# Optimization experiments

Hardware: AMD Instinct MI355X
Metric: run time of the kernel (lower is better)

The kernel has to match this reference:

```python
import jax, jax.numpy as jnp
import numpy as np

SHIFT = 1  # fixed instance of the random +/-1 shift_direction


def setup_inputs() -> dict:
    key = jax.random.key(0)
    k1, k2 = jax.random.split(key)
    x = jax.random.normal(k1, (128, 256, 28, 28), dtype=jnp.float32)
    W = jax.random.normal(k2, (128, 3, 128), dtype=jnp.float32)  # (j=in, k=3, i=out)
    return {"x": x, "W": W}


def reference(x, W):
    B, G, Cg, H, Wd = 128, 2, 128, 28, 28
    # view as (l, o, j, n, m) = (batch, group, chan, h, w)
    xg = x.reshape(B, G, Cg, H, Wd)
    # circular roll along width (original: roll(t, shift, dim=4))
    xg = jnp.roll(xg, SHIFT, axis=4)
    # unfold(3,1) pad (1,0) + einsum 'lojnmk, jki -> lonmi' is exactly a
    # zero-padded 1D conv along width with full channel mixing, shared over
    # group and h. Express it as a single grouped-batch conv.
    xm = xg.reshape(B * G, Cg, H, Wd)                 # (N, C, H, W)
    kern = jnp.transpose(W, (2, 0, 1))[:, :, None, :]  # (i, j, 1, 3) OIHW
    y = jax.lax.conv_general_dilated(
        xm, kern, window_strides=(1, 1), padding=((0, 0), (1, 1)),
        dimension_numbers=("NCHW", "OIHW", "NCHW"))   # (B*G, i, H, W)
    y = y.reshape(B, G, Cg, H, Wd)                    # (l, o, i, n, m)
    # second roll is along h (dim 1 of the (l,n,m,o*i) layout == n here)
    y = jnp.roll(y, SHIFT, axis=3)
    # final layout (l, o*i, n, m) == (128, 256, 28, 28)
    return y.reshape(B, G * Cg, H, Wd)
```

## Files before the change

kernel.cpp:

```cpp
#include <hip/hip_runtime.h>


typedef __bf16  bf16x8 __attribute__((ext_vector_type(8)));
typedef float  f32x16 __attribute__((ext_vector_type(16)));

__global__ __launch_bounds__(256, 2)
void shiftconv_kernel(const float* __restrict__ x,
                      const float* __restrict__ Wm,
                      float* __restrict__ out)
{
    __shared__ unsigned short xsp[34 * 128];

    const int tid  = threadIdx.x;
    const int wave = tid >> 6;
    const int lane = tid & 63;
    const int lo   = lane & 31;
    const int hi   = lane >> 5;

    const int b  = blockIdx.x;
    const int l  = b >> 3;
    const int o  = (b >> 2) & 1;
    const int nc = b & 3;

    bf16x8 bw[3][8];
    {
        const int i = wave * 32 + lo;
#pragma unroll
        for (int kw = 0; kw < 3; ++kw) {
#pragma unroll
            for (int jc = 0; jc < 8; ++jc) {
                const int j0 = jc * 16 + hi * 8;
#pragma unroll
                for (int e = 0; e < 8; ++e) {
                    bw[kw][jc][e] = (__bf16)Wm[(((j0 + e) * 3) + kw) * 128 + i];
                }
            }
        }
    }

    {
        const int rl[6] = {0, 29, 30, 31, 32, 33};
#pragma unroll
        for (int q = 0; q < 3; ++q) {
            const int e  = q * 256 + tid;
            const int rr = rl[e >> 7];
            const int j  = e & 127;
            xsp[rr * 128 + (j ^ ((rr & 7) << 3))] = 0;
        }
    }

    const float* xbase = x   + (size_t)(l * 256 + o * 128) * 784;
    float*       obase = out + (size_t)(l * 256 + o * 128) * 784;

    for (int n1 = nc * 7; n1 < nc * 7 + 7; ++n1) {
        __syncthreads();

        for (int g = tid; g < 896; g += 256) {
            const int j  = g / 7;
            const int mq = g - j * 7;
            const float4 v = *reinterpret_cast<const float4*>(
                xbase + j * 784 + n1 * 28 + mq * 4);
            const float vv[4] = {v.x, v.y, v.z, v.w};
#pragma unroll
            for (int e = 0; e < 4; ++e) {
                const int m = mq * 4 + e;
                const int r = (m == 27) ? 1 : (m + 2);
                union { __bf16 h; unsigned short u; } cv;
                cv.h = (__bf16)vv[e];
                xsp[r * 128 + (j ^ ((r & 7) << 3))] = cv.u;
            }
        }
        __syncthreads();

        f32x16 acc = {0,0,0,0, 0,0,0,0, 0,0,0,0, 0,0,0,0};
#pragma unroll
        for (int kw = 0; kw < 3; ++kw) {
#pragma unroll
            for (int jc = 0; jc < 8; ++jc) {
                const int row = kw + lo;
                const int j0  = jc * 16 + hi * 8;
                const bf16x8 a = *reinterpret_cast<const bf16x8*>(
                    &xsp[row * 128 + (j0 ^ ((row & 7) << 3))]);
                acc = __builtin_amdgcn_mfma_f32_32x32x16_bf16(a, bw[kw][jc], acc, 0, 0, 0);
            }
        }

        const int n = (n1 + 1) % 28;
        const int i = wave * 32 + lo;
        float* op = obase + (size_t)i * 784 + n * 28;
#pragma unroll
        for (int q = 0; q < 4; ++q) {
            const int m0 = 8 * q + 4 * hi;
            if (m0 <= 24) {
                float4 st = make_float4(acc[4*q+0], acc[4*q+1], acc[4*q+2], acc[4*q+3]);
                *reinterpret_cast<float4*>(op + m0) = st;
            }
        }
    }
}

extern "C" void kernel_launch(void* const* d_in, const int* in_sizes, int n_in,
                              void* d_out, int out_size, void* d_ws, size_t ws_size,
                              hipStream_t stream) {
    const float* x  = (const float*)d_in[0];
    const float* Wm = (const float*)d_in[1];
    float* out = (float*)d_out;
    hipLaunchKernelGGL(shiftconv_kernel, dim3(1024), dim3(256), 0, stream, x, Wm, out);
}
```

Baseline: 248.1 us.

## Double-buffer LDS with register prefetch and split MFMA into 16x16 tiles

Prefetches the next input row into registers while computing the current one, staging into a second LDS buffer to cut a barrier per row. Uses 8 waves with 16x16x32 bf16 MFMA so each wave owns 16 output channels, raising occupancy and spreading weight registers. Padding rows beyond 29 are left unzeroed, relying on their results never being stored.

```diff
diff --git a/kernel.cpp b/kernel.cpp
--- a/kernel.cpp
+++ b/kernel.cpp
@@ -1,101 +1,118 @@
 #include <hip/hip_runtime.h>
 
 
-typedef __bf16  bf16x8 __attribute__((ext_vector_type(8)));
-typedef float  f32x16 __attribute__((ext_vector_type(16)));
+typedef __bf16 bf16x8 __attribute__((ext_vector_type(8)));
+typedef float  f32x4  __attribute__((ext_vector_type(4)));
 
-__global__ __launch_bounds__(256, 2)
+__device__ __forceinline__ int swz(int r, int j) {
+    return r * 128 + (j ^ ((r & 7) << 3));
+}
+
+#define STAGE_WRITE(BUF, V, J, MQ)                                   \
+    {                                                                \
+        _Pragma("unroll")                                            \
+        for (int e = 0; e < 4; ++e) {                                \
+            const int m = (MQ) * 4 + e;                              \
+            const int r = (m == 27) ? 1 : (m + 2);                   \
+            union { __bf16 h; unsigned short u; } cv;                \
+            cv.h = (__bf16)((&(V).x)[e]);                            \
+            xsp[BUF][swz(r, (J))] = cv.u;                            \
+        }                                                            \
+    }
+
+__global__ __launch_bounds__(512, 4)
 void shiftconv_kernel(const float* __restrict__ x,
                       const float* __restrict__ Wm,
                       float* __restrict__ out)
 {
-    __shared__ unsigned short xsp[34 * 128];
+    __shared__ unsigned short xsp[2][34 * 128];
 
     const int tid  = threadIdx.x;
     const int wave = tid >> 6;
     const int lane = tid & 63;
-    const int lo   = lane & 31;
-    const int hi   = lane >> 5;
+    const int l15  = lane & 15;
+    const int hi2  = lane >> 4;
 
     const int b  = blockIdx.x;
     const int l  = b >> 3;
     const int o  = (b >> 2) & 1;
     const int nc = b & 3;
 
-    bf16x8 bw[3][8];
-    {
-        const int i = wave * 32 + lo;
+    const float* xbase = x   + (size_t)(l * 256 + o * 128) * 784;
+    float*       obase = out + (size_t)(l * 256 + o * 128) * 784;
+
+    const int ga  = tid;
+    const int gb  = tid + 512;
+    const int ja  = ga / 7,  ma = ga - ja * 7;
+    const int jb2 = gb / 7,  mb = gb - jb2 * 7;
+    const bool vb = (gb < 896);
+
+    int n1 = nc * 7;
+
+    float4 pa = *reinterpret_cast<const float4*>(xbase + ja * 784 + n1 * 28 + ma * 4);
+    float4 pb = make_float4(0.f, 0.f, 0.f, 0.f);
+    if (vb) pb = *reinterpret_cast<const float4*>(xbase + jb2 * 784 + n1 * 28 + mb * 4);
+
+    const int ig = wave * 16 + l15;
+    bf16x8 bw[12];
 #pragma unroll
-        for (int kw = 0; kw < 3; ++kw) {
+    for (int s = 0; s < 12; ++s) {
+        const int kw = s >> 2;
+        const int jb = (s & 3) * 32 + hi2 * 8;
 #pragma unroll
-            for (int jc = 0; jc < 8; ++jc) {
-                const int j0 = jc * 16 + hi * 8;
-#pragma unroll
-                for (int e = 0; e < 8; ++e) {
-                    bw[kw][jc][e] = (__bf16)Wm[(((j0 + e) * 3) + kw) * 128 + i];
-                }
-            }
-        }
+        for (int e = 0; e < 8; ++e)
+            bw[s][e] = (__bf16)Wm[((jb + e) * 3 + kw) * 128 + ig];
     }
 
     {
-        const int rl[6] = {0, 29, 30, 31, 32, 33};
-#pragma unroll
-        for (int q = 0; q < 3; ++q) {
-            const int e  = q * 256 + tid;
-            const int rr = rl[e >> 7];
-            const int j  = e & 127;
-            xsp[rr * 128 + (j ^ ((rr & 7) << 3))] = 0;
-        }
+        const int buf = tid >> 8;
+        const int r   = ((tid >> 7) & 1) ? 29 : 0;
+        const int j   = tid & 127;
+        xsp[buf][swz(r, j)] = 0;
     }
 
-    const float* xbase = x   + (size_t)(l * 256 + o * 128) * 784;
-    float*       obase = out + (size_t)(l * 256 + o * 128) * 784;
+    STAGE_WRITE(0, pa, ja, ma);
+    if (vb) STAGE_WRITE(0, pb, jb2, mb);
 
-    for (int n1 = nc * 7; n1 < nc * 7 + 7; ++n1) {
+    int cur = 0;
+#pragma unroll 1
+    for (int t = 0; t < 7; ++t) {
         __syncthreads();
 
-        for (int g = tid; g < 896; g += 256) {
-            const int j  = g / 7;
-            const int mq = g - j * 7;
-            const float4 v = *reinterpret_cast<const float4*>(
-                xbase + j * 784 + n1 * 28 + mq * 4);
-            const float vv[4] = {v.x, v.y, v.z, v.w};
+        float4 na, nb;
+        const bool more = (t < 6);
+        if (more) {
+            na = *reinterpret_cast<const float4*>(xbase + ja * 784 + (n1 + 1) * 28 + ma * 4);
+            if (vb) nb = *reinterpret_cast<const float4*>(xbase + jb2 * 784 + (n1 + 1) * 28 + mb * 4);
+        }
+
+        f32x4 acc0 = {0.f, 0.f, 0.f, 0.f};
+        f32x4 acc1 = {0.f, 0.f, 0.f, 0.f};
+        const unsigned short* xs = xsp[cur];
 #pragma unroll
-            for (int e = 0; e < 4; ++e) {
-                const int m = mq * 4 + e;
-                const int r = (m == 27) ? 1 : (m + 2);
-                union { __bf16 h; unsigned short u; } cv;
-                cv.h = (__bf16)vv[e];
-                xsp[r * 128 + (j ^ ((r & 7) << 3))] = cv.u;
-            }
-        }
-        __syncthreads();
-
-        f32x16 acc = {0,0,0,0, 0,0,0,0, 0,0,0,0, 0,0,0,0};
-#pragma unroll
-        for (int kw = 0; kw < 3; ++kw) {
-#pragma unroll
-            for (int jc = 0; jc < 8; ++jc) {
-                const int row = kw + lo;
-                const int j0  = jc * 16 + hi * 8;
-                const bf16x8 a = *reinterpret_cast<const bf16x8*>(
-                    &xsp[row * 128 + (j0 ^ ((row & 7) << 3))]);
-                acc = __builtin_amdgcn_mfma_f32_32x32x16_bf16(a, bw[kw][jc], acc, 0, 0, 0);
-            }
+        for (int s = 0; s < 12; ++s) {
+            const int kw = s >> 2;
+            const int jb = (s & 3) * 32 + hi2 * 8;
+            const bf16x8 a0 = *reinterpret_cast<const bf16x8*>(&xs[swz(l15 + kw, jb)]);
+            acc0 = __builtin_amdgcn_mfma_f32_16x16x32_bf16(a0, bw[s], acc0, 0, 0, 0);
+            const bf16x8 a1 = *reinterpret_cast<const bf16x8*>(&xs[swz(16 + l15 + kw, jb)]);
+            acc1 = __builtin_amdgcn_mfma_f32_16x16x32_bf16(a1, bw[s], acc1, 0, 0, 0);
         }
 
         const int n = (n1 + 1) % 28;
-        const int i = wave * 32 + lo;
-        float* op = obase + (size_t)i * 784 + n * 28;
-#pragma unroll
-        for (int q = 0; q < 4; ++q) {
-            const int m0 = 8 * q + 4 * hi;
-            if (m0 <= 24) {
-                float4 st = make_float4(acc[4*q+0], acc[4*q+1], acc[4*q+2], acc[4*q+3]);
-                *reinterpret_cast<float4*>(op + m0) = st;
-            }
+        float* op = obase + (size_t)ig * 784 + n * 28;
+        *reinterpret_cast<float4*>(op + hi2 * 4) =
+            make_float4(acc0[0], acc0[1], acc0[2], acc0[3]);
+        if (hi2 < 3)
+            *reinterpret_cast<float4*>(op + 16 + hi2 * 4) =
+                make_float4(acc1[0], acc1[1], acc1[2], acc1[3]);
+
+        if (more) {
+            STAGE_WRITE(cur ^ 1, na, ja, ma);
+            if (vb) STAGE_WRITE(cur ^ 1, nb, jb2, mb);
         }
+        cur ^= 1;
+        ++n1;
     }
 }
 
@@ -105,5 +122,5 @@
     const float* x  = (const float*)d_in[0];
     const float* Wm = (const float*)d_in[1];
     float* out = (float*)d_out;
-    hipLaunchKernelGGL(shiftconv_kernel, dim3(1024), dim3(256), 0, stream, x, Wm, out);
+    hipLaunchKernelGGL(shiftconv_kernel, dim3(1024), dim3(512), 0, stream, x, Wm, out);
 }
```

New measurement: 222.7 us. 1.11x faster.
